# Performance work log

Hardware: AMD Instinct MI355X
Metric: run time of the kernel (lower is better)

## Reference

```python
import jax, jax.numpy as jnp
import numpy as np

N = 8192
F_IN = 256
F_OUT = 128
ALPHA = 0.2  # leaky relu negative slope


def _leaky(x):
    return jnp.where(x >= 0, x, ALPHA * x)


def setup_inputs() -> dict:
    key = jax.random.key(0)
    ks = jax.random.split(key, 12)
    nodes = jax.random.normal(ks[0], (N, F_IN), dtype=jnp.float32)
    adj = (jax.random.uniform(ks[1], (N, N)) < 0.05).astype(jnp.float32)
    adj = jnp.maximum(adj, jnp.eye(N, dtype=jnp.float32))
    s = 0.02
    W1 = jax.random.normal(ks[2], (F_IN, F_OUT), dtype=jnp.float32) * s
    b1 = jnp.zeros((F_OUT,), jnp.float32)
    W2 = jax.random.normal(ks[3], (F_OUT, F_OUT), dtype=jnp.float32) * s
    b2 = jnp.zeros((F_OUT,), jnp.float32)
    W3 = jax.random.normal(ks[4], (F_OUT, F_OUT), dtype=jnp.float32) * s
    b3 = jnp.zeros((F_OUT,), jnp.float32)
    W4 = jax.random.normal(ks[5], (F_OUT, F_OUT), dtype=jnp.float32) * s
    b4 = jnp.zeros((F_OUT,), jnp.float32)
    a_w = jax.random.normal(ks[6], (2 * F_OUT,), dtype=jnp.float32) * s
    a_b = jnp.zeros((), jnp.float32)
    return {"nodes": nodes, "adj": adj, "W1": W1, "b1": b1, "W2": W2, "b2": b2,
            "W3": W3, "b3": b3, "W4": W4, "b4": b4, "a_w": a_w, "a_b": a_b}


def reference(nodes, adj, W1, b1, W2, b2, W3, b3, W4, b4, a_w, a_b):
    # 4-layer linear stack
    h = jax.nn.relu(nodes @ W1 + b1)
    h = jax.nn.relu(h @ W2 + b2)
    h = jax.nn.relu(h @ W3 + b3)
    h = h @ W4 + b4  # (N, F_OUT)
    # a([h_i, h_j]) is linear -> split into src/dst components instead of
    # materializing the (N, N, 2F) repeat+cat tensor; identical math.
    a1, a2 = a_w[:F_OUT], a_w[F_OUT:]
    s_src = h @ a1  # (N,)
    s_dst = h @ a2  # (N,)
    e = _leaky(s_src[:, None] + s_dst[None, :] + a_b)  # (N, N)
    e = jnp.where(adj >= 0.5, e, -jnp.inf)
    attention = jax.nn.softmax(e, axis=1)
    # dropout is identity in eval mode
    return _leaky(attention @ h)  # (N, F_OUT)
```

## Files before the change

kernel.cpp:

```cpp
#include <hip/hip_runtime.h>
#include <hip/hip_bf16.h>

#define N_NODES 8192
#define F_IN    256
#define F_OUT   128
#define WCAP    576

typedef float f4v __attribute__((ext_vector_type(4)));
typedef unsigned int u32;

__device__ __forceinline__ float leaky(float x) { return x >= 0.f ? x : 0.2f * x; }
__device__ __forceinline__ u32 bf16rn(float a) {
  const u32 u = __float_as_uint(a);
  return (u + 0x7FFFu + ((u >> 16) & 1u)) >> 16;
}
__device__ __forceinline__ u32 packbf(float a, float b) {
  return bf16rn(a) | (bf16rn(b) << 16);
}
__device__ __forceinline__ float bflo(u32 u) { return __uint_as_float(u << 16); }
__device__ __forceinline__ float bfhi(u32 u) { return __uint_as_float(u & 0xFFFF0000u); }

#define WAVE_LDS (8 * 256 + 8 * 128 + 8 * 128)

__device__ __forceinline__ void mlp_step4(const float* hbase, int stride, int k0,
                                          const float2 w[4], float acc[8][2]) {
#pragma unroll
  for (int r = 0; r < 8; ++r) {
    const float4 h4 = *(const float4*)(hbase + r * stride + k0);
    acc[r][0] += h4.x * w[0].x; acc[r][1] += h4.x * w[0].y;
    acc[r][0] += h4.y * w[1].x; acc[r][1] += h4.y * w[1].y;
    acc[r][0] += h4.z * w[2].x; acc[r][1] += h4.z * w[2].y;
    acc[r][0] += h4.w * w[3].x; acc[r][1] += h4.w * w[3].y;
  }
}

template <int K, int STRIDE>
__device__ __forceinline__ void mlp_layer(const float* __restrict__ W, int n0,
                                          const float* hbase, float acc[8][2]) {
#pragma unroll
  for (int r = 0; r < 8; ++r) { acc[r][0] = 0.f; acc[r][1] = 0.f; }
  float2 wA[4], wB[4];
#pragma unroll
  for (int kk = 0; kk < 4; ++kk)
    wA[kk] = *(const float2*)(W + (size_t)kk * F_OUT + n0);
#pragma unroll 1
  for (int k8 = 0; k8 < K / 8; ++k8) {
    const int kb = k8 * 8;
#pragma unroll
    for (int kk = 0; kk < 4; ++kk)
      wB[kk] = *(const float2*)(W + (size_t)(kb + 4 + kk) * F_OUT + n0);
    mlp_step4(hbase, STRIDE, kb, wA, acc);
    if (k8 + 1 < K / 8) {
#pragma unroll
      for (int kk = 0; kk < 4; ++kk)
        wA[kk] = *(const float2*)(W + (size_t)(kb + 8 + kk) * F_OUT + n0);
    }
    mlp_step4(hbase, STRIDE, kb + 4, wB, acc);
  }
}

__global__ __launch_bounds__(256) void mlp_fused(
    const float* __restrict__ nodes,
    const float* __restrict__ W1, const float* __restrict__ b1,
    const float* __restrict__ W2, const float* __restrict__ b2,
    const float* __restrict__ W3, const float* __restrict__ b3,
    const float* __restrict__ W4, const float* __restrict__ b4,
    const float* __restrict__ aw,
    u32* __restrict__ hb_out, float* __restrict__ ss, float* __restrict__ sd) {
  __shared__ float lds[4][WAVE_LDS];

  const int tid = threadIdx.x;
  const int w = tid >> 6;
  const int l = tid & 63;
  const int row0 = blockIdx.x * 32 + w * 8;
  const int n0 = 2 * l;

  float* A  = &lds[w][0];
  float* h1 = &lds[w][2048];
  float* h2 = &lds[w][2048 + 1024];

#pragma unroll
  for (int r = 0; r < 8; ++r) {
    const float4 v = *(const float4*)(nodes + (size_t)(row0 + r) * F_IN + l * 4);
    *(float4*)&A[r * 256 + l * 4] = v;
  }

  float acc[8][2];

  mlp_layer<256, 256>(W1, n0, A, acc);
  {
    const float2 bv = *(const float2*)(b1 + n0);
#pragma unroll
    for (int r = 0; r < 8; ++r) {
      float2 o = {fmaxf(acc[r][0] + bv.x, 0.f), fmaxf(acc[r][1] + bv.y, 0.f)};
      *(float2*)&h1[r * 128 + n0] = o;
    }
  }
  mlp_layer<128, 128>(W2, n0, h1, acc);
  {
    const float2 bv = *(const float2*)(b2 + n0);
#pragma unroll
    for (int r = 0; r < 8; ++r) {
      float2 o = {fmaxf(acc[r][0] + bv.x, 0.f), fmaxf(acc[r][1] + bv.y, 0.f)};
      *(float2*)&h2[r * 128 + n0] = o;
    }
  }
  mlp_layer<128, 128>(W3, n0, h2, acc);
  {
    const float2 bv = *(const float2*)(b3 + n0);
#pragma unroll
    for (int r = 0; r < 8; ++r) {
      float2 o = {fmaxf(acc[r][0] + bv.x, 0.f), fmaxf(acc[r][1] + bv.y, 0.f)};
      *(float2*)&h1[r * 128 + n0] = o;
    }
  }
  mlp_layer<128, 128>(W4, n0, h1, acc);
  {
    const float2 bv = *(const float2*)(b4 + n0);
#pragma unroll
    for (int r = 0; r < 8; ++r) { acc[r][0] += bv.x; acc[r][1] += bv.y; }
  }

  const float2 a1v = *(const float2*)(aw + n0);
  const float2 a2v = *(const float2*)(aw + F_OUT + n0);
#pragma unroll
  for (int r = 0; r < 8; ++r) {
    hb_out[(size_t)(row0 + r) * 64 + l] = packbf(acc[r][0], acc[r][1]);
    float s1 = acc[r][0] * a1v.x + acc[r][1] * a1v.y;
    float s2 = acc[r][0] * a2v.x + acc[r][1] * a2v.y;
#pragma unroll
    for (int o = 1; o < 64; o <<= 1) {
      s1 += __shfl_xor(s1, o, 64);
      s2 += __shfl_xor(s2, o, 64);
    }
    if (l == 0) { ss[row0 + r] = s1; sd[row0 + r] = s2; }
  }
}

__global__ __launch_bounds__(256) void attn_wave(const float* __restrict__ adj,
                                                 const u32* __restrict__ hb,
                                                 const float* __restrict__ s_src,
                                                 const float* __restrict__ s_dst,
                                                 const float* __restrict__ ab_ptr,
                                                 float* __restrict__ out) {
  __shared__ float2 lst[4][WCAP];

  const int tid = threadIdx.x;
  const int w = tid >> 6;
  const int lane = tid & 63;
  const int row = blockIdx.x * 4 + w;
  float2* lc = lst[w];

  const float sbase = s_src[row] + ab_ptr[0];
  const f4v* arow = (const f4v*)(adj + (size_t)row * N_NODES);
  const float4* sd4 = (const float4*)s_dst;
  const uint4* hb4 = (const uint4*)hb;
  const unsigned long long lt = (1ull << lane) - 1ull;

  f4v av = __builtin_nontemporal_load(arow + lane);
  float4 sv = sd4[lane];
  int base = 0;
  float lsum = 0.f;

#pragma unroll 2
  for (int it = 0; it < 32; ++it) {
    const f4v av_c = av;
    const float4 sv_c = sv;
    if (it + 1 < 32) {
      av = __builtin_nontemporal_load(arow + (it + 1) * 64 + lane);
      sv = sd4[(it + 1) * 64 + lane];
    }
    const bool hx = av_c.x >= 0.5f, hy = av_c.y >= 0.5f, hz = av_c.z >= 0.5f, hw = av_c.w >= 0.5f;
    const unsigned long long m0 = __ballot(hx);
    const unsigned long long m1 = __ballot(hy);
    const unsigned long long m2 = __ballot(hz);
    const unsigned long long m3 = __ballot(hw);
    const int t0 = __popcll(m0), t1 = __popcll(m1), t2 = __popcll(m2), t3 = __popcll(m3);
    const int j0 = (it * 64 + lane) * 4;
    if (hx) {
      const int p = base + __popcll(m0 & lt);
      if (p < WCAP) { const float ww = __expf(leaky(sbase + sv_c.x)); lc[p] = make_float2(ww, __int_as_float(j0)); lsum += ww; }
    }
    if (hy) {
      const int p = base + t0 + __popcll(m1 & lt);
      if (p < WCAP) { const float ww = __expf(leaky(sbase + sv_c.y)); lc[p] = make_float2(ww, __int_as_float(j0 + 1)); lsum += ww; }
    }
    if (hz) {
      const int p = base + t0 + t1 + __popcll(m2 & lt);
      if (p < WCAP) { const float ww = __expf(leaky(sbase + sv_c.z)); lc[p] = make_float2(ww, __int_as_float(j0 + 2)); lsum += ww; }
    }
    if (hw) {
      const int p = base + t0 + t1 + t2 + __popcll(m3 & lt);
      if (p < WCAP) { const float ww = __expf(leaky(sbase + sv_c.w)); lc[p] = make_float2(ww, __int_as_float(j0 + 3)); lsum += ww; }
    }
    base += t0 + t1 + t2 + t3;
  }

  const int n = (base < WCAP) ? base : WCAP;
  const int g4 = lane >> 4;
  const int q = lane & 15;
  float accv[8] = {};
#pragma unroll 4
  for (int p = g4; p < n; p += 4) {
    const float2 pr = lc[p];
    const uint4 hv = hb4[(size_t)__float_as_int(pr.y) * 16 + q];
    accv[0] += pr.x * bflo(hv.x); accv[1] += pr.x * bfhi(hv.x);
    accv[2] += pr.x * bflo(hv.y); accv[3] += pr.x * bfhi(hv.y);
    accv[4] += pr.x * bflo(hv.z); accv[5] += pr.x * bfhi(hv.z);
    accv[6] += pr.x * bflo(hv.w); accv[7] += pr.x * bfhi(hv.w);
  }

#pragma unroll
  for (int e = 0; e < 8; ++e) {
    accv[e] += __shfl_xor(accv[e], 16, 64);
    accv[e] += __shfl_xor(accv[e], 32, 64);
  }
#pragma unroll
  for (int o = 1; o < 64; o <<= 1) lsum += __shfl_xor(lsum, o, 64);

  if (lane < 16) {
    const float inv = 1.f / lsum;
    float4 o0, o1;
    o0.x = leaky(accv[0] * inv); o0.y = leaky(accv[1] * inv);
    o0.z = leaky(accv[2] * inv); o0.w = leaky(accv[3] * inv);
    o1.x = leaky(accv[4] * inv); o1.y = leaky(accv[5] * inv);
    o1.z = leaky(accv[6] * inv); o1.w = leaky(accv[7] * inv);
    ((float4*)out)[(size_t)row * 32 + q * 2]     = o0;
    ((float4*)out)[(size_t)row * 32 + q * 2 + 1] = o1;
  }
}

extern "C" void kernel_launch(void* const* d_in, const int* in_sizes, int n_in,
                              void* d_out, int out_size, void* d_ws, size_t ws_size,
                              hipStream_t stream) {
  const float* nodes = (const float*)d_in[0];
  const float* adj   = (const float*)d_in[1];
  const float* W1    = (const float*)d_in[2];
  const float* b1    = (const float*)d_in[3];
  const float* W2    = (const float*)d_in[4];
  const float* b2    = (const float*)d_in[5];
  const float* W3    = (const float*)d_in[6];
  const float* b3    = (const float*)d_in[7];
  const float* W4    = (const float*)d_in[8];
  const float* b4    = (const float*)d_in[9];
  const float* aw    = (const float*)d_in[10];
  const float* ab    = (const float*)d_in[11];
  float* out = (float*)d_out;

  u32*  hb = (u32*)d_ws;
  float* ss = (float*)((char*)d_ws + (size_t)N_NODES * F_OUT * 2);
  float* sd = ss + N_NODES;

  mlp_fused<<<N_NODES / 32, 256, 0, stream>>>(nodes, W1, b1, W2, b2, W3, b3,
                                              W4, b4, aw, hb, ss, sd);
  attn_wave<<<N_NODES / 4, 256, 0, stream>>>(adj, hb, ss, sd, ab, out);
}
```

Baseline: 465.6 us.

## Split attention into separate adjacency-scan and neighbor-gather kernels via global list

```diff
diff --git a/kernel.cpp b/kernel.cpp
--- a/kernel.cpp
+++ b/kernel.cpp
@@ -137,24 +137,22 @@
   }
 }
 
-__global__ __launch_bounds__(256) void attn_wave(const float* __restrict__ adj,
-                                                 const u32* __restrict__ hb,
+__global__ __launch_bounds__(256) void attn_scan(const float* __restrict__ adj,
                                                  const float* __restrict__ s_src,
                                                  const float* __restrict__ s_dst,
                                                  const float* __restrict__ ab_ptr,
-                                                 float* __restrict__ out) {
-  __shared__ float2 lst[4][WCAP];
-
+                                                 float2* __restrict__ glist,
+                                                 int* __restrict__ gcnt,
+                                                 float* __restrict__ gwsum) {
   const int tid = threadIdx.x;
   const int w = tid >> 6;
   const int lane = tid & 63;
   const int row = blockIdx.x * 4 + w;
-  float2* lc = lst[w];
+  float2* lc = glist + (size_t)row * WCAP;
 
   const float sbase = s_src[row] + ab_ptr[0];
   const f4v* arow = (const f4v*)(adj + (size_t)row * N_NODES);
   const float4* sd4 = (const float4*)s_dst;
-  const uint4* hb4 = (const uint4*)hb;
   const unsigned long long lt = (1ull << lane) - 1ull;
 
   f4v av = __builtin_nontemporal_load(arow + lane);
@@ -196,9 +194,31 @@
     base += t0 + t1 + t2 + t3;
   }
 
-  const int n = (base < WCAP) ? base : WCAP;
+#pragma unroll
+  for (int o = 1; o < 64; o <<= 1) lsum += __shfl_xor(lsum, o, 64);
+  if (lane == 0) {
+    gcnt[row] = base;
+    gwsum[row] = lsum;
+  }
+}
+
+__global__ __launch_bounds__(256) void attn_gather(const u32* __restrict__ hb,
+                                                   const float2* __restrict__ glist,
+                                                   const int* __restrict__ gcnt,
+                                                   const float* __restrict__ gwsum,
+                                                   float* __restrict__ out) {
+  const int tid = threadIdx.x;
+  const int w = tid >> 6;
+  const int lane = tid & 63;
+  const int row = blockIdx.x * 4 + w;
+  const float2* lc = glist + (size_t)row * WCAP;
+  const uint4* hb4 = (const uint4*)hb;
+
+  const int cntv = gcnt[row];
+  const int n = (cntv < WCAP) ? cntv : WCAP;
   const int g4 = lane >> 4;
   const int q = lane & 15;
+
   float accv[8] = {};
 #pragma unroll 4
   for (int p = g4; p < n; p += 4) {
@@ -215,11 +235,9 @@
     accv[e] += __shfl_xor(accv[e], 16, 64);
     accv[e] += __shfl_xor(accv[e], 32, 64);
   }
-#pragma unroll
-  for (int o = 1; o < 64; o <<= 1) lsum += __shfl_xor(lsum, o, 64);
 
   if (lane < 16) {
-    const float inv = 1.f / lsum;
+    const float inv = 1.f / gwsum[row];
     float4 o0, o1;
     o0.x = leaky(accv[0] * inv); o0.y = leaky(accv[1] * inv);
     o0.z = leaky(accv[2] * inv); o0.w = leaky(accv[3] * inv);
@@ -247,11 +265,16 @@
   const float* ab    = (const float*)d_in[11];
   float* out = (float*)d_out;
 
-  u32*  hb = (u32*)d_ws;
-  float* ss = (float*)((char*)d_ws + (size_t)N_NODES * F_OUT * 2);
-  float* sd = ss + N_NODES;
+  char* wsb = (char*)d_ws;
+  u32*    hb    = (u32*)wsb;
+  float*  ss    = (float*)(wsb + (size_t)N_NODES * F_OUT * 2);
+  float*  sd    = ss + N_NODES;
+  int*    gcnt  = (int*)(sd + N_NODES);
+  float*  gwsum = (float*)(gcnt + N_NODES);
+  float2* glist = (float2*)(gwsum + N_NODES);
 
   mlp_fused<<<N_NODES / 32, 256, 0, stream>>>(nodes, W1, b1, W2, b2, W3, b3,
                                               W4, b4, aw, hb, ss, sd);
-  attn_wave<<<N_NODES / 4, 256, 0, stream>>>(adj, hb, ss, sd, ab, out);
-}
+  attn_scan<<<N_NODES / 4, 256, 0, stream>>>(adj, ss, sd, ab, glist, gcnt, gwsum);
+  attn_gather<<<N_NODES / 4, 256, 0, stream>>>(hb, glist, gcnt, gwsum, out);
+}
```

Result: slower. 499.3 us (+7.2%).

## Interleave adjacency compaction with weighted gather per chunk

Applied to the files above, without the earlier changes.

```diff
diff --git a/kernel.cpp b/kernel.cpp
--- a/kernel.cpp
+++ b/kernel.cpp
@@ -137,89 +137,91 @@
   }
 }
 
+__device__ __forceinline__ void compact4(const f4v v, int j0, int& base,
+                                         unsigned long long lt, int* lc) {
+  const bool hx = v.x >= 0.5f, hy = v.y >= 0.5f, hz = v.z >= 0.5f, hw = v.w >= 0.5f;
+  const unsigned long long m0 = __ballot(hx);
+  const unsigned long long m1 = __ballot(hy);
+  const unsigned long long m2 = __ballot(hz);
+  const unsigned long long m3 = __ballot(hw);
+  const int t0 = __popcll(m0), t1 = __popcll(m1), t2 = __popcll(m2), t3 = __popcll(m3);
+  if (hx) { const int p = base + __popcll(m0 & lt);                if (p < WCAP) lc[p] = j0; }
+  if (hy) { const int p = base + t0 + __popcll(m1 & lt);           if (p < WCAP) lc[p] = j0 + 1; }
+  if (hz) { const int p = base + t0 + t1 + __popcll(m2 & lt);      if (p < WCAP) lc[p] = j0 + 2; }
+  if (hw) { const int p = base + t0 + t1 + t2 + __popcll(m3 & lt); if (p < WCAP) lc[p] = j0 + 3; }
+  base += t0 + t1 + t2 + t3;
+}
+
 __global__ __launch_bounds__(256) void attn_wave(const float* __restrict__ adj,
                                                  const u32* __restrict__ hb,
                                                  const float* __restrict__ s_src,
                                                  const float* __restrict__ s_dst,
                                                  const float* __restrict__ ab_ptr,
                                                  float* __restrict__ out) {
-  __shared__ float2 lst[4][WCAP];
+  __shared__ int lst[4][WCAP];
 
   const int tid = threadIdx.x;
   const int w = tid >> 6;
   const int lane = tid & 63;
   const int row = blockIdx.x * 4 + w;
-  float2* lc = lst[w];
+  int* lc = lst[w];
 
   const float sbase = s_src[row] + ab_ptr[0];
   const f4v* arow = (const f4v*)(adj + (size_t)row * N_NODES);
-  const float4* sd4 = (const float4*)s_dst;
   const uint4* hb4 = (const uint4*)hb;
   const unsigned long long lt = (1ull << lane) - 1ull;
-
-  f4v av = __builtin_nontemporal_load(arow + lane);
-  float4 sv = sd4[lane];
-  int base = 0;
-  float lsum = 0.f;
-
-#pragma unroll 2
-  for (int it = 0; it < 32; ++it) {
-    const f4v av_c = av;
-    const float4 sv_c = sv;
-    if (it + 1 < 32) {
-      av = __builtin_nontemporal_load(arow + (it + 1) * 64 + lane);
-      sv = sd4[(it + 1) * 64 + lane];
-    }
-    const bool hx = av_c.x >= 0.5f, hy = av_c.y >= 0.5f, hz = av_c.z >= 0.5f, hw = av_c.w >= 0.5f;
-    const unsigned long long m0 = __ballot(hx);
-    const unsigned long long m1 = __ballot(hy);
-    const unsigned long long m2 = __ballot(hz);
-    const unsigned long long m3 = __ballot(hw);
-    const int t0 = __popcll(m0), t1 = __popcll(m1), t2 = __popcll(m2), t3 = __popcll(m3);
-    const int j0 = (it * 64 + lane) * 4;
-    if (hx) {
-      const int p = base + __popcll(m0 & lt);
-      if (p < WCAP) { const float ww = __expf(leaky(sbase + sv_c.x)); lc[p] = make_float2(ww, __int_as_float(j0)); lsum += ww; }
-    }
-    if (hy) {
-      const int p = base + t0 + __popcll(m1 & lt);
-      if (p < WCAP) { const float ww = __expf(leaky(sbase + sv_c.y)); lc[p] = make_float2(ww, __int_as_float(j0 + 1)); lsum += ww; }
-    }
-    if (hz) {
-      const int p = base + t0 + t1 + __popcll(m2 & lt);
-      if (p < WCAP) { const float ww = __expf(leaky(sbase + sv_c.z)); lc[p] = make_float2(ww, __int_as_float(j0 + 2)); lsum += ww; }
-    }
-    if (hw) {
-      const int p = base + t0 + t1 + t2 + __popcll(m3 & lt);
-      if (p < WCAP) { const float ww = __expf(leaky(sbase + sv_c.w)); lc[p] = make_float2(ww, __int_as_float(j0 + 3)); lsum += ww; }
-    }
-    base += t0 + t1 + t2 + t3;
-  }
-
-  const int n = (base < WCAP) ? base : WCAP;
   const int g4 = lane >> 4;
   const int q = lane & 15;
+
+  f4v a0 = __builtin_nontemporal_load(arow + lane);
+  f4v a1 = __builtin_nontemporal_load(arow + 64 + lane);
+  f4v a2 = __builtin_nontemporal_load(arow + 128 + lane);
+  f4v a3 = __builtin_nontemporal_load(arow + 192 + lane);
+
+  int base = 0;
+  float ws = 0.f;
   float accv[8] = {};
-#pragma unroll 4
-  for (int p = g4; p < n; p += 4) {
-    const float2 pr = lc[p];
-    const uint4 hv = hb4[(size_t)__float_as_int(pr.y) * 16 + q];
-    accv[0] += pr.x * bflo(hv.x); accv[1] += pr.x * bfhi(hv.x);
-    accv[2] += pr.x * bflo(hv.y); accv[3] += pr.x * bfhi(hv.y);
-    accv[4] += pr.x * bflo(hv.z); accv[5] += pr.x * bfhi(hv.z);
-    accv[6] += pr.x * bflo(hv.w); accv[7] += pr.x * bfhi(hv.w);
-  }
-
-#pragma unroll
-  for (int e = 0; e < 8; ++e) {
-    accv[e] += __shfl_xor(accv[e], 16, 64);
-    accv[e] += __shfl_xor(accv[e], 32, 64);
-  }
-#pragma unroll
-  for (int o = 1; o < 64; o <<= 1) lsum += __shfl_xor(lsum, o, 64);
+
+#pragma unroll 1
+  for (int c = 0; c < 8; ++c) {
+    const f4v c0 = a0, c1 = a1, c2 = a2, c3 = a3;
+    if (c + 1 < 8) {
+      const int o = (c + 1) * 256 + lane;
+      a0 = __builtin_nontemporal_load(arow + o);
+      a1 = __builtin_nontemporal_load(arow + o + 64);
+      a2 = __builtin_nontemporal_load(arow + o + 128);
+      a3 = __builtin_nontemporal_load(arow + o + 192);
+    }
+    const int gstart = base;
+    const int jb = c * 1024 + lane * 4;
+    compact4(c0, jb,        base, lt, lc);
+    compact4(c1, jb + 256,  base, lt, lc);
+    compact4(c2, jb + 512,  base, lt, lc);
+    compact4(c3, jb + 768,  base, lt, lc);
+
+    const int e = (base < WCAP) ? base : WCAP;
+    for (int p = gstart + g4; p < e; p += 4) {
+      const int j = lc[p];
+      const float wgt = __expf(leaky(sbase + s_dst[j]));
+      const uint4 hv = hb4[(size_t)j * 16 + q];
+      ws += wgt;
+      accv[0] += wgt * bflo(hv.x); accv[1] += wgt * bfhi(hv.x);
+      accv[2] += wgt * bflo(hv.y); accv[3] += wgt * bfhi(hv.y);
+      accv[4] += wgt * bflo(hv.z); accv[5] += wgt * bfhi(hv.z);
+      accv[6] += wgt * bflo(hv.w); accv[7] += wgt * bfhi(hv.w);
+    }
+  }
+
+#pragma unroll
+  for (int e2 = 0; e2 < 8; ++e2) {
+    accv[e2] += __shfl_xor(accv[e2], 16, 64);
+    accv[e2] += __shfl_xor(accv[e2], 32, 64);
+  }
+  ws += __shfl_xor(ws, 16, 64);
+  ws += __shfl_xor(ws, 32, 64);
 
   if (lane < 16) {
-    const float inv = 1.f / lsum;
+    const float inv = 1.f / ws;
     float4 o0, o1;
     o0.x = leaky(accv[0] * inv); o0.y = leaky(accv[1] * inv);
     o0.z = leaky(accv[2] * inv); o0.w = leaky(accv[3] * inv);
```

Result: no change. 469.7 us (+0.9%).
